# Kernel tuning notes

Measured on AMD Instinct MI355X. Metric: run time of the kernel, lower is better.

Reference implementation:

```python
import jax, jax.numpy as jnp
import numpy as np

B, T, C = 4, 2048, 1024
H, D = 16, 64
SCALE = D ** -0.5


def setup_inputs() -> dict:
    key = jax.random.key(0)
    ks = jax.random.split(key, 5)
    s = 0.02
    return {
        "hidden_states": jax.random.normal(ks[0], (B, T, C), dtype=jnp.float32),
        "attention_mask": jnp.ones((B, T), dtype=jnp.int32),
        "Wq": jax.random.normal(ks[1], (C, H * D), dtype=jnp.float32) * s,
        "Wk": jax.random.normal(ks[2], (C, H * D), dtype=jnp.float32) * s,
        "Wv": jax.random.normal(ks[3], (C, H * D), dtype=jnp.float32) * s,
        "Wo": jax.random.normal(ks[4], (H * D, C), dtype=jnp.float32) * s,
        "bo": jnp.zeros((C,), dtype=jnp.float32),
    }


def reference(hidden_states, attention_mask, Wq, Wk, Wv, Wo, bo):
    b, t, _ = hidden_states.shape
    # projections -> (B, H, T, D)
    q = (hidden_states @ Wq).reshape(b, t, H, D).transpose(0, 2, 1, 3)
    k = (hidden_states @ Wk).reshape(b, t, H, D).transpose(0, 2, 1, 3)
    v = (hidden_states @ Wv).reshape(b, t, H, D).transpose(0, 2, 1, 3)
    # scores (B, H, Tq, Tk)
    scores = jnp.einsum("bhqd,bhkd->bhqk", q, k) * SCALE
    mask = attention_mask[:, None, None, :]  # (B,1,1,T), dim==2 branch
    scores = jnp.where(mask == 0, -jnp.inf, scores)
    probs = jax.nn.softmax(scores, axis=-1)
    out = jnp.einsum("bhqk,bhkd->bhqd", probs, v)
    out = out.transpose(0, 2, 1, 3).reshape(b, t, H * D)
    return out @ Wo + bo
```

## Files before the change

kernel.cpp:

```cpp
#include <hip/hip_runtime.h>
#include <hip/hip_bf16.h>

#define B_ 4
#define T_ 2048
#define C_ 1024
#define H_ 16
#define D_ 64
#define SCALE_ 0.125f
#define L2E 1.4426950408889634f
#define SE (SCALE_ * L2E)

typedef __attribute__((ext_vector_type(8))) short bf16x8;
typedef __attribute__((ext_vector_type(4))) float f32x4;

__device__ __forceinline__ unsigned short f2bf(float f) {
    union { float f; unsigned u; } v; v.f = f;
    unsigned r = v.u + 0x7fff + ((v.u >> 16) & 1);
    return (unsigned short)(r >> 16);
}

__device__ __forceinline__ unsigned pk2bf(float a, float b) {
    __hip_bfloat162 t = __float22bfloat162_rn(make_float2(a, b));
    union { __hip_bfloat162 h; unsigned u; } c; c.h = t;
    return c.u;
}

__device__ __forceinline__ void gl_lds16(const unsigned short* g, unsigned short* l) {
    __builtin_amdgcn_global_load_lds(
        (const __attribute__((address_space(1))) void*)g,
        (__attribute__((address_space(3))) void*)l,
        16, 0, 0);
}

__global__ void cvt_hs_kernel(const float4* __restrict__ in, ushort4* __restrict__ out) {
    int i = blockIdx.x * 256 + threadIdx.x;
    float4 v = in[i];
    ushort4 o;
    o.x = f2bf(v.x); o.y = f2bf(v.y); o.z = f2bf(v.z); o.w = f2bf(v.w);
    out[i] = o;
}

__global__ void wtrans_kernel(const float* __restrict__ Wq, const float* __restrict__ Wk,
                              const float* __restrict__ Wv, const float* __restrict__ Wo,
                              unsigned short* __restrict__ Wqkv_t, unsigned short* __restrict__ Wo_t) {
    __shared__ float tile[64][65];
    int mtx = blockIdx.y;
    const float* W = (mtx == 0) ? Wq : (mtx == 1) ? Wk : (mtx == 2) ? Wv : Wo;
    unsigned short* Out = (mtx < 3) ? (Wqkv_t + (size_t)mtx * 1024 * 1024) : Wo_t;
    int tl = blockIdx.x;
    int tx = tl & 15, ty = tl >> 4;
    int t = threadIdx.x;
    int col = t & 63, rb = t >> 6;
#pragma unroll
    for (int rr = 0; rr < 16; ++rr) {
        int r = rb * 16 + rr;
        tile[r][col] = W[(size_t)(ty * 64 + r) * 1024 + tx * 64 + col];
    }
    __syncthreads();
#pragma unroll
    for (int rr = 0; rr < 16; ++rr) {
        int r = rb * 16 + rr;
        Out[(size_t)(tx * 64 + r) * 1024 + ty * 64 + col] = f2bf(tile[col][r]);
    }
}

__global__ __launch_bounds__(256) void gemm_qkv_kernel(
    const unsigned short* __restrict__ A, const unsigned short* __restrict__ Bt,
    unsigned short* __restrict__ Qg, unsigned short* __restrict__ Kf, unsigned short* __restrict__ Vf) {
    __shared__ __align__(16) unsigned short As[128 * 32];
    __shared__ __align__(16) unsigned short Bs[128 * 32];
    const int tid = threadIdx.x;
    const int w = tid >> 6, lane = tid & 63;
    const int quad = lane >> 4, l16 = lane & 15;
    const int m0 = blockIdx.y * 128, n0 = blockIdx.x * 128;
    const int mw = (w >> 1) * 64, nw = (w & 1) * 64;
    const int K = 1024;
    const int srow = lane >> 2;
    const int scol = (lane & 3) * 8;

    const f32x4 fzero = {0.f, 0.f, 0.f, 0.f};
    f32x4 acc[4][4];
#pragma unroll
    for (int i = 0; i < 4; ++i)
#pragma unroll
        for (int j = 0; j < 4; ++j) acc[i][j] = fzero;

    for (int k0 = 0; k0 < K; k0 += 32) {
        gl_lds16(A + (size_t)(m0 + w * 32 + srow) * K + k0 + scol,       As + (w * 32) * 32);
        gl_lds16(A + (size_t)(m0 + w * 32 + 16 + srow) * K + k0 + scol,  As + (w * 32 + 16) * 32);
        gl_lds16(Bt + (size_t)(n0 + w * 32 + srow) * K + k0 + scol,      Bs + (w * 32) * 32);
        gl_lds16(Bt + (size_t)(n0 + w * 32 + 16 + srow) * K + k0 + scol, Bs + (w * 32 + 16) * 32);
        __syncthreads();
        bf16x8 a[4], b[4];
#pragma unroll
        for (int i = 0; i < 4; ++i)
            a[i] = *(const bf16x8*)(As + (mw + i * 16 + l16) * 32 + quad * 8);
#pragma unroll
        for (int j = 0; j < 4; ++j)
            b[j] = *(const bf16x8*)(Bs + (nw + j * 16 + l16) * 32 + quad * 8);
#pragma unroll
        for (int i = 0; i < 4; ++i)
#pragma unroll
            for (int j = 0; j < 4; ++j)
                acc[i][j] = __builtin_amdgcn_mfma_f32_16x16x32_bf16(a[i], b[j], acc[i][j], 0, 0, 0);
        __syncthreads();
    }

#pragma unroll
    for (int j = 0; j < 4; ++j) {
        int gn = n0 + nw + j * 16 + l16;
        int tensor = gn >> 10;
        int nl = gn & 1023;
        int hh = nl >> 6, dd = nl & 63;
#pragma unroll
        for (int i = 0; i < 4; ++i) {
            int gmb = m0 + mw + i * 16 + quad * 4;
            int bb = gmb >> 11;
            size_t bhh = (size_t)(bb * 16 + hh);
            if (tensor == 0) {
#pragma unroll
                for (int r = 0; r < 4; ++r) {
                    int tt = (gmb + r) & 2047;
                    Qg[(bhh * 2048 + tt) * 64 + dd] = f2bf(acc[i][j][r] * SE);
                }
            } else if (tensor == 1) {
#pragma unroll
                for (int r = 0; r < 4; ++r) {
                    int tt = (gmb + r) & 2047;
                    Kf[bhh * 131072 + (size_t)(tt >> 4) * 1024 + (dd >> 5) * 512 +
                       (((dd >> 3) & 3) * 16 + (tt & 15)) * 8 + (dd & 7)] = f2bf(acc[i][j][r]);
                }
            } else {
                int tt = gmb & 2047;
                ushort4 v4;
                v4.x = f2bf(acc[i][j][0]); v4.y = f2bf(acc[i][j][1]);
                v4.z = f2bf(acc[i][j][2]); v4.w = f2bf(acc[i][j][3]);
                *(ushort4*)(Vf + bhh * 131072 + (size_t)(tt >> 5) * 2048 + (dd >> 4) * 512 +
                            (((tt >> 3) & 3) * 16 + (dd & 15)) * 8 + (tt & 7)) = v4;
            }
        }
    }
}

__device__ __forceinline__ void attn_step_staged(
    int k0, const unsigned short* Kc, const unsigned short* Vc,
    unsigned short* Kn, unsigned short* Vn, int kn0,
    const unsigned short* __restrict__ Kg, const unsigned short* __restrict__ Vg,
    unsigned short* Pw, const bf16x8 (&aq)[2][2], const bf16x8& vones,
    f32x4 (&po)[2][4], f32x4 (&pl)[2],
    const int* __restrict__ mrow, int w, int lane, int quad, int l16) {

    gl_lds16(Kg + (size_t)(kn0 >> 4) * 1024 + w * 512 + lane * 8, Kn + w * 512);
    gl_lds16(Vg + (size_t)(kn0 >> 5) * 2048 + w * 512 + lane * 8, Vn + w * 512);

    bf16x8 ka0[4], ka1[4];
#pragma unroll
    for (int kt = 0; kt < 4; ++kt) {
        ka0[kt] = *(const bf16x8*)(Kc + kt * 1024 + lane * 8);
        ka1[kt] = *(const bf16x8*)(Kc + kt * 1024 + 512 + lane * 8);
    }

    const f32x4 fzero = {0.f, 0.f, 0.f, 0.f};
    int mk = mrow[k0 + lane];
    bool allok = (__ballot(mk != 0) == 0xFFFFFFFFFFFFFFFFull);

    if (allok) {
#pragma unroll
        for (int kt = 0; kt < 4; ++kt) {
            int pidx = ((((kt & 1) << 1) | (quad >> 1)) * 16 + l16) * 8 + (quad & 1) * 4;
#pragma unroll
            for (int qi = 0; qi < 2; ++qi) {
                f32x4 st = __builtin_amdgcn_mfma_f32_16x16x32_bf16(ka0[kt], aq[qi][0], fzero, 0, 0, 0);
                st = __builtin_amdgcn_mfma_f32_16x16x32_bf16(ka1[kt], aq[qi][1], st, 0, 0, 0);
                float p0 = __builtin_amdgcn_exp2f(st[0]);
                float p1 = __builtin_amdgcn_exp2f(st[1]);
                float p2 = __builtin_amdgcn_exp2f(st[2]);
                float p3 = __builtin_amdgcn_exp2f(st[3]);
                uint2 pk; pk.x = pk2bf(p0, p1); pk.y = pk2bf(p2, p3);
                *(uint2*)(Pw + (qi * 2 + (kt >> 1)) * 512 + pidx) = pk;
            }
        }
    } else {
#pragma unroll
        for (int kt = 0; kt < 4; ++kt) {
            int4 mv = *(const int4*)(mrow + k0 + kt * 16 + quad * 4);
            float mb0 = mv.x ? 0.f : -1e30f;
            float mb1 = mv.y ? 0.f : -1e30f;
            float mb2 = mv.z ? 0.f : -1e30f;
            float mb3 = mv.w ? 0.f : -1e30f;
            int pidx = ((((kt & 1) << 1) | (quad >> 1)) * 16 + l16) * 8 + (quad & 1) * 4;
#pragma unroll
            for (int qi = 0; qi < 2; ++qi) {
                f32x4 st = __builtin_amdgcn_mfma_f32_16x16x32_bf16(ka0[kt], aq[qi][0], fzero, 0, 0, 0);
                st = __builtin_amdgcn_mfma_f32_16x16x32_bf16(ka1[kt], aq[qi][1], st, 0, 0, 0);
                float p0 = __builtin_amdgcn_exp2f(st[0] + mb0);
                float p1 = __builtin_amdgcn_exp2f(st[1] + mb1);
                float p2 = __builtin_amdgcn_exp2f(st[2] + mb2);
                float p3 = __builtin_amdgcn_exp2f(st[3] + mb3);
                uint2 pk; pk.x = pk2bf(p0, p1); pk.y = pk2bf(p2, p3);
                *(uint2*)(Pw + (qi * 2 + (kt >> 1)) * 512 + pidx) = pk;
            }
        }
    }

    bf16x8 bv[2][4];
#pragma unroll
    for (int c = 0; c < 2; ++c)
#pragma unroll
        for (int nd = 0; nd < 4; ++nd)
            bv[c][nd] = *(const bf16x8*)(Vc + c * 2048 + nd * 512 + lane * 8);

    asm volatile("s_waitcnt lgkmcnt(0)" ::: "memory");

#pragma unroll
    for (int c = 0; c < 2; ++c)
#pragma unroll
        for (int qi = 0; qi < 2; ++qi) {
            bf16x8 ap = *(const bf16x8*)(Pw + (qi * 2 + c) * 512 + lane * 8);
#pragma unroll
            for (int nd = 0; nd < 4; ++nd)
                po[qi][nd] = __builtin_amdgcn_mfma_f32_16x16x32_bf16(ap, bv[c][nd], po[qi][nd], 0, 0, 0);
            pl[qi] = __builtin_amdgcn_mfma_f32_16x16x32_bf16(ap, vones, pl[qi], 0, 0, 0);
        }
}

__global__ __launch_bounds__(512, 4) void attn_kernel(
    const unsigned short* __restrict__ Qg, const unsigned short* __restrict__ Kf,
    const unsigned short* __restrict__ Vf, const int* __restrict__ mask,
    unsigned short* __restrict__ AO) {
    __shared__ __align__(16) unsigned short KsA[4096], KsB[4096];
    __shared__ __align__(16) unsigned short VsA[4096], VsB[4096];
    __shared__ __align__(16) unsigned short Pbuf[8][2048];

    const int tid = threadIdx.x;
    const int w = tid >> 6, lane = tid & 63;
    const int quad = lane >> 4, l16 = lane & 15;
    const int bid = blockIdx.x;
    const int bh = (bid & 7) * 8 + ((bid >> 6) & 7);
    const int qt = (bid >> 3) & 7;
    const int b = bh >> 4, h = bh & 15;
    const size_t bh_td = (size_t)bh * (2048 * 64);
    const int q0w = qt * 256 + w * 32;

    bf16x8 aq[2][2];
#pragma unroll
    for (int qi = 0; qi < 2; ++qi)
#pragma unroll
        for (int hh = 0; hh < 2; ++hh)
            aq[qi][hh] = *(const bf16x8*)(Qg + bh_td + (size_t)(q0w + qi * 16 + l16) * 64 + hh * 32 + quad * 8);

    const unsigned short* Kg = Kf + bh_td;
    const unsigned short* Vg = Vf + bh_td;
    const int* mrow = mask + b * 2048;

    bf16x8 vones;
#pragma unroll
    for (int i = 0; i < 8; ++i) vones[i] = (short)0x3F80;

    const f32x4 fzero = {0.f, 0.f, 0.f, 0.f};
    f32x4 po[2][4];
    f32x4 pl[2];
#pragma unroll
    for (int qi = 0; qi < 2; ++qi) {
        pl[qi] = fzero;
#pragma unroll
        for (int nd = 0; nd < 4; ++nd) po[qi][nd] = fzero;
    }

    gl_lds16(Kg + w * 512 + lane * 8, KsA + w * 512);
    gl_lds16(Vg + w * 512 + lane * 8, VsA + w * 512);
    asm volatile("s_waitcnt vmcnt(0)" ::: "memory");
    __syncthreads();

#pragma unroll 1
    for (int k0 = 0; k0 < 2048; k0 += 128) {
        attn_step_staged(k0, KsA, VsA, KsB, VsB, k0 + 64,
                         Kg, Vg, Pbuf[w], aq, vones, po, pl, mrow, w, lane, quad, l16);
        asm volatile("s_waitcnt vmcnt(0)" ::: "memory");
        __syncthreads();
        attn_step_staged(k0 + 64, KsB, VsB, KsA, VsA, (k0 + 128) & 2047,
                         Kg, Vg, Pbuf[w], aq, vones, po, pl, mrow, w, lane, quad, l16);
        asm volatile("s_waitcnt vmcnt(0)" ::: "memory");
        __syncthreads();
    }

#pragma unroll
    for (int qi = 0; qi < 2; ++qi)
#pragma unroll
        for (int r = 0; r < 4; ++r) {
            float linv = __builtin_amdgcn_rcpf(pl[qi][r]);
            int q = q0w + qi * 16 + quad * 4 + r;
            size_t ob = (size_t)(b * 2048 + q) * 1024 + h * 64;
#pragma unroll
            for (int nd = 0; nd < 4; ++nd)
                AO[ob + nd * 16 + l16] = f2bf(po[qi][nd][r] * linv);
        }
}

__global__ __launch_bounds__(256) void gemm_out_kernel(
    const unsigned short* __restrict__ A, const unsigned short* __restrict__ Bt,
    const float* __restrict__ bo, float* __restrict__ out) {
    __shared__ __align__(16) unsigned short As[128 * 32];
    __shared__ __align__(16) unsigned short Bs[128 * 32];
    const int tid = threadIdx.x;
    const int w = tid >> 6, lane = tid & 63;
    const int quad = lane >> 4, l16 = lane & 15;
    const int m0 = blockIdx.y * 128, n0 = blockIdx.x * 128;
    const int mw = (w >> 1) * 64, nw = (w & 1) * 64;
    const int K = 1024;
    const int srow = lane >> 2;
    const int scol = (lane & 3) * 8;

    const f32x4 fzero = {0.f, 0.f, 0.f, 0.f};
    f32x4 acc[4][4];
#pragma unroll
    for (int i = 0; i < 4; ++i)
#pragma unroll
        for (int j = 0; j < 4; ++j) acc[i][j] = fzero;

    for (int k0 = 0; k0 < K; k0 += 32) {
        gl_lds16(A + (size_t)(m0 + w * 32 + srow) * K + k0 + scol,       As + (w * 32) * 32);
        gl_lds16(A + (size_t)(m0 + w * 32 + 16 + srow) * K + k0 + scol,  As + (w * 32 + 16) * 32);
        gl_lds16(Bt + (size_t)(n0 + w * 32 + srow) * K + k0 + scol,      Bs + (w * 32) * 32);
        gl_lds16(Bt + (size_t)(n0 + w * 32 + 16 + srow) * K + k0 + scol, Bs + (w * 32 + 16) * 32);
        __syncthreads();
        bf16x8 a[4], b[4];
#pragma unroll
    for (int i = 0; i < 4; ++i)
            a[i] = *(const bf16x8*)(As + (mw + i * 16 + l16) * 32 + quad * 8);
#pragma unroll
        for (int j = 0; j < 4; ++j)
            b[j] = *(const bf16x8*)(Bs + (nw + j * 16 + l16) * 32 + quad * 8);
#pragma unroll
        for (int i = 0; i < 4; ++i)
#pragma unroll
            for (int j = 0; j < 4; ++j)
                acc[i][j] = __builtin_amdgcn_mfma_f32_16x16x32_bf16(a[i], b[j], acc[i][j], 0, 0, 0);
        __syncthreads();
    }

#pragma unroll
    for (int j = 0; j < 4; ++j) {
        int gn = n0 + nw + j * 16 + l16;
        float bias = bo[gn];
#pragma unroll
        for (int i = 0; i < 4; ++i) {
            int gmb = m0 + mw + i * 16 + quad * 4;
#pragma unroll
            for (int r = 0; r < 4; ++r)
                out[(size_t)(gmb + r) * 1024 + gn] = acc[i][j][r] + bias;
        }
    }
}

extern "C" void kernel_launch(void* const* d_in, const int* in_sizes, int n_in,
                              void* d_out, int out_size, void* d_ws, size_t ws_size,
                              hipStream_t stream) {
    const float* hs  = (const float*)d_in[0];
    const int* mask  = (const int*)d_in[1];
    const float* Wq  = (const float*)d_in[2];
    const float* Wk  = (const float*)d_in[3];
    const float* Wv  = (const float*)d_in[4];
    const float* Wo  = (const float*)d_in[5];
    const float* bo  = (const float*)d_in[6];
    float* out = (float*)d_out;

    char* ws = (char*)d_ws;
    unsigned short* hs_bf = (unsigned short*)(ws);
    unsigned short* wqkv  = (unsigned short*)(ws + 16777216);
    unsigned short* wo_t  = (unsigned short*)(ws + 23068672);
    unsigned short* Qg    = (unsigned short*)(ws + 25165824);
    unsigned short* Kf    = (unsigned short*)(ws + 41943040);
    unsigned short* Vf    = (unsigned short*)(ws + 58720256);
    unsigned short* AO    = (unsigned short*)(ws + 75497472);

    cvt_hs_kernel<<<8192, 256, 0, stream>>>((const float4*)hs, (ushort4*)hs_bf);
    wtrans_kernel<<<dim3(256, 4), 256, 0, stream>>>(Wq, Wk, Wv, Wo, wqkv, wo_t);
    gemm_qkv_kernel<<<dim3(24, 64), 256, 0, stream>>>(hs_bf, wqkv, Qg, Kf, Vf);
    attn_kernel<<<512, 512, 0, stream>>>(Qg, Kf, Vf, mask, AO);
    gemm_out_kernel<<<dim3(8, 64), 256, 0, stream>>>(AO, wo_t, bo, out);
}
```

Baseline: 279.5 us.

## Merge conversion kernels and double GEMM K-tile to 64

The hidden-state bf16 conversion and the weight transpose/convert kernels are merged into one launch that picks its role by block index, removing one kernel launch and its gap. Both projection GEMMs now stage a 64-wide K slice per iteration instead of 32, running two MFMA sub-steps per barrier pair. This halves the number of synchronizations and global-to-LDS rounds. The cost is doubled LDS per block, which may reduce occupancy, and rows of 64 bf16 may cause more LDS bank conflicts on the fragment reads.

```diff
diff --git a/kernel.cpp b/kernel.cpp
--- a/kernel.cpp
+++ b/kernel.cpp
@@ -32,25 +32,28 @@
         16, 0, 0);
 }
 
-__global__ void cvt_hs_kernel(const float4* __restrict__ in, ushort4* __restrict__ out) {
-    int i = blockIdx.x * 256 + threadIdx.x;
-    float4 v = in[i];
-    ushort4 o;
-    o.x = f2bf(v.x); o.y = f2bf(v.y); o.z = f2bf(v.z); o.w = f2bf(v.w);
-    out[i] = o;
-}
-
-__global__ void wtrans_kernel(const float* __restrict__ Wq, const float* __restrict__ Wk,
-                              const float* __restrict__ Wv, const float* __restrict__ Wo,
-                              unsigned short* __restrict__ Wqkv_t, unsigned short* __restrict__ Wo_t) {
+__global__ void cvtw_kernel(const float4* __restrict__ in, ushort4* __restrict__ out,
+                            const float* __restrict__ Wq, const float* __restrict__ Wk,
+                            const float* __restrict__ Wv, const float* __restrict__ Wo,
+                            unsigned short* __restrict__ Wqkv_t, unsigned short* __restrict__ Wo_t) {
     __shared__ float tile[64][65];
-    int mtx = blockIdx.y;
+    const int bid = blockIdx.x;
+    const int t = threadIdx.x;
+    if (bid < 8192) {
+        int i = bid * 256 + t;
+        float4 v = in[i];
+        ushort4 o;
+        o.x = f2bf(v.x); o.y = f2bf(v.y); o.z = f2bf(v.z); o.w = f2bf(v.w);
+        out[i] = o;
+        return;
+    }
+    const int wb = bid - 8192;
+    const int mtx = wb >> 8;
     const float* W = (mtx == 0) ? Wq : (mtx == 1) ? Wk : (mtx == 2) ? Wv : Wo;
     unsigned short* Out = (mtx < 3) ? (Wqkv_t + (size_t)mtx * 1024 * 1024) : Wo_t;
-    int tl = blockIdx.x;
-    int tx = tl & 15, ty = tl >> 4;
-    int t = threadIdx.x;
-    int col = t & 63, rb = t >> 6;
+    const int tl = wb & 255;
+    const int tx = tl & 15, ty = tl >> 4;
+    const int col = t & 63, rb = t >> 6;
 #pragma unroll
     for (int rr = 0; rr < 16; ++rr) {
         int r = rb * 16 + rr;
@@ -67,16 +70,16 @@
 __global__ __launch_bounds__(256) void gemm_qkv_kernel(
     const unsigned short* __restrict__ A, const unsigned short* __restrict__ Bt,
     unsigned short* __restrict__ Qg, unsigned short* __restrict__ Kf, unsigned short* __restrict__ Vf) {
-    __shared__ __align__(16) unsigned short As[128 * 32];
-    __shared__ __align__(16) unsigned short Bs[128 * 32];
+    __shared__ __align__(16) unsigned short As[128 * 64];
+    __shared__ __align__(16) unsigned short Bs[128 * 64];
     const int tid = threadIdx.x;
     const int w = tid >> 6, lane = tid & 63;
     const int quad = lane >> 4, l16 = lane & 15;
     const int m0 = blockIdx.y * 128, n0 = blockIdx.x * 128;
     const int mw = (w >> 1) * 64, nw = (w & 1) * 64;
     const int K = 1024;
-    const int srow = lane >> 2;
-    const int scol = (lane & 3) * 8;
+    const int srow = lane >> 3;
+    const int scol = (lane & 7) * 8;
 
     const f32x4 fzero = {0.f, 0.f, 0.f, 0.f};
     f32x4 acc[4][4];
@@ -85,24 +88,29 @@
 #pragma unroll
         for (int j = 0; j < 4; ++j) acc[i][j] = fzero;
 
-    for (int k0 = 0; k0 < K; k0 += 32) {
-        gl_lds16(A + (size_t)(m0 + w * 32 + srow) * K + k0 + scol,       As + (w * 32) * 32);
-        gl_lds16(A + (size_t)(m0 + w * 32 + 16 + srow) * K + k0 + scol,  As + (w * 32 + 16) * 32);
-        gl_lds16(Bt + (size_t)(n0 + w * 32 + srow) * K + k0 + scol,      Bs + (w * 32) * 32);
-        gl_lds16(Bt + (size_t)(n0 + w * 32 + 16 + srow) * K + k0 + scol, Bs + (w * 32 + 16) * 32);
-        __syncthreads();
-        bf16x8 a[4], b[4];
-#pragma unroll
-        for (int i = 0; i < 4; ++i)
-            a[i] = *(const bf16x8*)(As + (mw + i * 16 + l16) * 32 + quad * 8);
-#pragma unroll
-        for (int j = 0; j < 4; ++j)
-            b[j] = *(const bf16x8*)(Bs + (nw + j * 16 + l16) * 32 + quad * 8);
-#pragma unroll
-        for (int i = 0; i < 4; ++i)
+#pragma unroll 1
+    for (int k0 = 0; k0 < K; k0 += 64) {
+#pragma unroll
+        for (int g = 0; g < 4; ++g) {
+            gl_lds16(A + (size_t)(m0 + w * 32 + g * 8 + srow) * K + k0 + scol,  As + (w * 32 + g * 8) * 64);
+            gl_lds16(Bt + (size_t)(n0 + w * 32 + g * 8 + srow) * K + k0 + scol, Bs + (w * 32 + g * 8) * 64);
+        }
+        __syncthreads();
+#pragma unroll
+        for (int ks = 0; ks < 2; ++ks) {
+            bf16x8 a[4], b[4];
+#pragma unroll
+            for (int i = 0; i < 4; ++i)
+                a[i] = *(const bf16x8*)(As + (mw + i * 16 + l16) * 64 + ks * 32 + quad * 8);
 #pragma unroll
             for (int j = 0; j < 4; ++j)
-                acc[i][j] = __builtin_amdgcn_mfma_f32_16x16x32_bf16(a[i], b[j], acc[i][j], 0, 0, 0);
+                b[j] = *(const bf16x8*)(Bs + (nw + j * 16 + l16) * 64 + ks * 32 + quad * 8);
+#pragma unroll
+            for (int i = 0; i < 4; ++i)
+#pragma unroll
+                for (int j = 0; j < 4; ++j)
+                    acc[i][j] = __builtin_amdgcn_mfma_f32_16x16x32_bf16(a[i], b[j], acc[i][j], 0, 0, 0);
+        }
         __syncthreads();
     }
 
@@ -300,16 +308,16 @@
 __global__ __launch_bounds__(256) void gemm_out_kernel(
     const unsigned short* __restrict__ A, const unsigned short* __restrict__ Bt,
     const float* __restrict__ bo, float* __restrict__ out) {
-    __shared__ __align__(16) unsigned short As[128 * 32];
-    __shared__ __align__(16) unsigned short Bs[128 * 32];
+    __shared__ __align__(16) unsigned short As[128 * 64];
+    __shared__ __align__(16) unsigned short Bs[128 * 64];
     const int tid = threadIdx.x;
     const int w = tid >> 6, lane = tid & 63;
     const int quad = lane >> 4, l16 = lane & 15;
     const int m0 = blockIdx.y * 128, n0 = blockIdx.x * 128;
     const int mw = (w >> 1) * 64, nw = (w & 1) * 64;
     const int K = 1024;
-    const int srow = lane >> 2;
-    const int scol = (lane & 3) * 8;
+    const int srow = lane >> 3;
+    const int scol = (lane & 7) * 8;
 
     const f32x4 fzero = {0.f, 0.f, 0.f, 0.f};
     f32x4 acc[4][4];
@@ -318,24 +326,29 @@
 #pragma unroll
         for (int j = 0; j < 4; ++j) acc[i][j] = fzero;
 
-    for (int k0 = 0; k0 < K; k0 += 32) {
-        gl_lds16(A + (size_t)(m0 + w * 32 + srow) * K + k0 + scol,       As + (w * 32) * 32);
-        gl_lds16(A + (size_t)(m0 + w * 32 + 16 + srow) * K + k0 + scol,  As + (w * 32 + 16) * 32);
-        gl_lds16(Bt + (size_t)(n0 + w * 32 + srow) * K + k0 + scol,      Bs + (w * 32) * 32);
-        gl_lds16(Bt + (size_t)(n0 + w * 32 + 16 + srow) * K + k0 + scol, Bs + (w * 32 + 16) * 32);
-        __syncthreads();
-        bf16x8 a[4], b[4];
-#pragma unroll
-    for (int i = 0; i < 4; ++i)
-            a[i] = *(const bf16x8*)(As + (mw + i * 16 + l16) * 32 + quad * 8);
-#pragma unroll
-        for (int j = 0; j < 4; ++j)
-            b[j] = *(const bf16x8*)(Bs + (nw + j * 16 + l16) * 32 + quad * 8);
-#pragma unroll
-        for (int i = 0; i < 4; ++i)
+#pragma unroll 1
+    for (int k0 = 0; k0 < K; k0 += 64) {
+#pragma unroll
+        for (int g = 0; g < 4; ++g) {
+            gl_lds16(A + (size_t)(m0 + w * 32 + g * 8 + srow) * K + k0 + scol,  As + (w * 32 + g * 8) * 64);
+            gl_lds16(Bt + (size_t)(n0 + w * 32 + g * 8 + srow) * K + k0 + scol, Bs + (w * 32 + g * 8) * 64);
+        }
+        __syncthreads();
+#pragma unroll
+        for (int ks = 0; ks < 2; ++ks) {
+            bf16x8 a[4], b[4];
+#pragma unroll
+            for (int i = 0; i < 4; ++i)
+                a[i] = *(const bf16x8*)(As + (mw + i * 16 + l16) * 64 + ks * 32 + quad * 8);
 #pragma unroll
             for (int j = 0; j < 4; ++j)
-                acc[i][j] = __builtin_amdgcn_mfma_f32_16x16x32_bf16(a[i], b[j], acc[i][j], 0, 0, 0);
+                b[j] = *(const bf16x8*)(Bs + (nw + j * 16 + l16) * 64 + ks * 32 + quad * 8);
+#pragma unroll
+            for (int i = 0; i < 4; ++i)
+#pragma unroll
+                for (int j = 0; j < 4; ++j)
+                    acc[i][j] = __builtin_amdgcn_mfma_f32_16x16x32_bf16(a[i], b[j], acc[i][j], 0, 0, 0);
+        }
         __syncthreads();
     }
 
@@ -374,8 +387,8 @@
     unsigned short* Vf    = (unsigned short*)(ws + 58720256);
     unsigned short* AO    = (unsigned short*)(ws + 75497472);
 
-    cvt_hs_kernel<<<8192, 256, 0, stream>>>((const float4*)hs, (ushort4*)hs_bf);
-    wtrans_kernel<<<dim3(256, 4), 256, 0, stream>>>(Wq, Wk, Wv, Wo, wqkv, wo_t);
+    cvtw_kernel<<<9216, 256, 0, stream>>>((const float4*)hs, (ushort4*)hs_bf,
+                                          Wq, Wk, Wv, Wo, wqkv, wo_t);
     gemm_qkv_kernel<<<dim3(24, 64), 256, 0, stream>>>(hs_bf, wqkv, Qg, Kf, Vf);
     attn_kernel<<<512, 512, 0, stream>>>(Qg, Kf, Vf, mask, AO);
     gemm_out_kernel<<<dim3(8, 64), 256, 0, stream>>>(AO, wo_t, bo, out);
```

Result: no change. 281.7 us (+0.8%).
